# Kernel optimization log

Hardware: AMD Instinct MI355X
Metric: run time of the kernel (lower is better)

Reference implementation:

```python
import jax, jax.numpy as jnp
import numpy as np

HIDDEN = 2048
N_HEADS = 16
HEAD_DIM = HIDDEN // N_HEADS
SEQ = 4096
ROPE_BASE = 10000.0


def setup_inputs() -> dict:
    key = jax.random.key(0)
    ks = jax.random.split(key, 5)
    sc = 1.0 / np.sqrt(HIDDEN)
    return {
        "hidden_states": jax.random.normal(ks[0], (SEQ, HIDDEN), jnp.float32),
        "Wq": jax.random.normal(ks[1], (HIDDEN, HIDDEN), jnp.float32) * sc,
        "Wk": jax.random.normal(ks[2], (HIDDEN, HIDDEN), jnp.float32) * sc,
        "Wv": jax.random.normal(ks[3], (HIDDEN, HIDDEN), jnp.float32) * sc,
        "Wo": jax.random.normal(ks[4], (HIDDEN, HIDDEN), jnp.float32) * sc,
    }


def _rope_cos_sin(seq_len, head_dim, dtype):
    # Llama-style rotary embedding tables, shape [S, 1, head_dim]
    inv_freq = 1.0 / (ROPE_BASE ** (jnp.arange(0, head_dim, 2, dtype=jnp.float32) / head_dim))
    pos = jnp.arange(seq_len, dtype=jnp.float32)
    freqs = pos[:, None] * inv_freq[None, :]          # [S, d/2]
    emb = jnp.concatenate([freqs, freqs], axis=-1)     # [S, d]
    return jnp.cos(emb)[:, None, :].astype(dtype), jnp.sin(emb)[:, None, :].astype(dtype)


def _rotate_half(x):
    h = x.shape[-1] // 2
    return jnp.concatenate([-x[..., h:], x[..., :h]], axis=-1)


def reference(hidden_states, Wq, Wk, Wv, Wo):
    S, H = hidden_states.shape
    d = HEAD_DIM
    # QKV projections (nn.Linear: x @ W.T), split into heads: [S, nH, d]
    q = (hidden_states @ Wq.T).reshape(S, N_HEADS, d)
    k = (hidden_states @ Wk.T).reshape(S, N_HEADS, d)
    v = (hidden_states @ Wv.T).reshape(S, N_HEADS, d)
    # Per-position RoPE on q and k
    cos, sin = _rope_cos_sin(S, d, q.dtype)
    q = q * cos + _rotate_half(q) * sin
    k = k * cos + _rotate_half(k) * sin
    # Causal scaled-dot-product attention, scores [nH, S, S]
    scores = jnp.einsum("snd,tnd->nst", q, k) / jnp.sqrt(jnp.asarray(d, q.dtype))
    causal = jnp.tril(jnp.ones((S, S), dtype=bool))
    scores = jnp.where(causal[None, :, :], scores, jnp.asarray(-1e30, scores.dtype))
    probs = jax.nn.softmax(scores, axis=-1)
    ctx = jnp.einsum("nst,tnd->snd", probs, v).reshape(S, H)
    return ctx @ Wo.T
```

## Files before the change

### kernel.cpp

```cpp
#include <hip/hip_runtime.h>

#define SEQ 4096
#define HIDDEN 2048
#define NHEADS 16
#define HDIM 128
#define QBLK 128
#define WQ 32
#define KVB 64

typedef float f32x4 __attribute__((ext_vector_type(4)));
typedef __bf16 bf16x8 __attribute__((ext_vector_type(8)));
typedef unsigned int u32x4 __attribute__((ext_vector_type(4)));
typedef unsigned int u32x2 __attribute__((ext_vector_type(2)));
typedef unsigned short u16x8 __attribute__((ext_vector_type(8)));
typedef unsigned short u16x4 __attribute__((ext_vector_type(4)));
typedef unsigned short u16;

#define SCL2 0.12751747456918851f
#define RLOG 0.2076205059304601f

__device__ __forceinline__ u16 f2bf(float f) {
  unsigned u = __float_as_uint(f);
  unsigned r = 0x7fffu + ((u >> 16) & 1u);
  return (u16)((u + r) >> 16);
}
__device__ __forceinline__ unsigned cvtpk(float a, float b) {
  unsigned r;
  asm volatile("v_cvt_pk_bf16_f32 %0, %1, %2" : "=v"(r) : "v"(a), "v"(b));
  return r;
}

__device__ __forceinline__ void gload16(const u16* g, u16* l) {
  __builtin_amdgcn_global_load_lds(
      (const __attribute__((address_space(1))) unsigned int*)g,
      (__attribute__((address_space(3))) unsigned int*)l, 16, 0, 0);
}

__global__ __launch_bounds__(256) void cvt5(const float* __restrict__ X,
    const float* __restrict__ Wq, const float* __restrict__ Wk,
    const float* __restrict__ Wv, const float* __restrict__ Wo,
    u16* __restrict__ dst) {
  const size_t SH = (size_t)SEQ * HIDDEN, HH = (size_t)HIDDEN * HIDDEN;
  size_t i = ((size_t)blockIdx.x * 256 + threadIdx.x) * 8;
  const float* src; size_t off;
  if (i < SH) { src = X; off = i; }
  else if (i < SH + HH) { src = Wq; off = i - SH; }
  else if (i < SH + 2 * HH) { src = Wk; off = i - SH - HH; }
  else if (i < SH + 3 * HH) { src = Wv; off = i - SH - 2 * HH; }
  else { src = Wo; off = i - SH - 3 * HH; }
  float4 a = *reinterpret_cast<const float4*>(src + off);
  float4 b = *reinterpret_cast<const float4*>(src + off + 4);
  u16x8 o;
  o[0] = f2bf(a.x); o[1] = f2bf(a.y); o[2] = f2bf(a.z); o[3] = f2bf(a.w);
  o[4] = f2bf(b.x); o[5] = f2bf(b.y); o[6] = f2bf(b.z); o[7] = f2bf(b.w);
  *reinterpret_cast<u32x4*>(dst + i) = __builtin_bit_cast(u32x4, o);
}

__global__ __launch_bounds__(256, 3) void gemm_qkv(const u16* __restrict__ Xb,
    const u16* __restrict__ Wqb, const u16* __restrict__ Wkb,
    const u16* __restrict__ Wvb, u16* __restrict__ Qo, u16* __restrict__ Ko,
    u16* __restrict__ Vt) {
  __shared__ u16 As[2][128 * 32];
  __shared__ u16 Bs[2][128 * 32];
  const int wg = blockIdx.x;
  const int swz = (wg & 7) * 192 + (wg >> 3);
  const int z = swz >> 9;
  const int rr_ = swz & 511;
  const u16 *A, *B;
  u16* C;
  int bm, bn, cst;
  if (z == 2) {
    A = Wvb; B = Xb; C = Vt;
    bm = (rr_ & 15) << 7; bn = (rr_ >> 4) << 7; cst = SEQ;
  } else {
    A = Xb; B = z ? Wkb : Wqb; C = z ? Ko : Qo;
    bm = (rr_ & 31) << 7; bn = (rr_ >> 5) << 7; cst = HIDDEN;
  }
  const int t = threadIdx.x, lane = t & 63, wave = t >> 6;
  const int lrow = lane & 15, lk = (lane >> 4) * 8;
  const int wr = wave * 32;
  const int r0 = t >> 2, c0 = (t & 3) * 8;

  f32x4 acc[2][8] = {};

#pragma unroll
  for (int is = 0; is < 2; ++is) {
    gload16(A + (size_t)(bm + is * 64 + r0) * HIDDEN + c0, &As[0][is * 2048 + t * 8]);
    gload16(B + (size_t)(bn + is * 64 + r0) * HIDDEN + c0, &Bs[0][is * 2048 + t * 8]);
  }
  __syncthreads();

  int p = 0;
  for (int kt = 0; kt < HIDDEN; kt += 32) {
    if (kt + 32 < HIDDEN) {
#pragma unroll
      for (int is = 0; is < 2; ++is) {
        gload16(A + (size_t)(bm + is * 64 + r0) * HIDDEN + kt + 32 + c0,
                &As[p ^ 1][is * 2048 + t * 8]);
        gload16(B + (size_t)(bn + is * 64 + r0) * HIDDEN + kt + 32 + c0,
                &Bs[p ^ 1][is * 2048 + t * 8]);
      }
    }
    bf16x8 af[2], bfv[8];
#pragma unroll
    for (int m = 0; m < 2; ++m)
      af[m] = __builtin_bit_cast(bf16x8,
          *reinterpret_cast<const u32x4*>(&As[p][(wr + m * 16 + lrow) * 32 + lk]));
#pragma unroll
    for (int n = 0; n < 8; ++n)
      bfv[n] = __builtin_bit_cast(bf16x8,
          *reinterpret_cast<const u32x4*>(&Bs[p][(n * 16 + lrow) * 32 + lk]));
#pragma unroll
    for (int n = 0; n < 8; ++n)
#pragma unroll
      for (int m = 0; m < 2; ++m)
        acc[m][n] = __builtin_amdgcn_mfma_f32_16x16x32_bf16(af[m], bfv[n], acc[m][n], 0, 0, 0);
    __syncthreads();
    p ^= 1;
  }

  const int rb = (lane >> 4) * 4;
  if (z < 2) {
#pragma unroll
    for (int m = 0; m < 2; ++m)
#pragma unroll
      for (int q = 0; q < 4; ++q) {
        const int s = bm + wr + m * 16 + rb + q;
#pragma unroll
        for (int n = 0; n < 4; ++n) {
          const int ii = n * 16 + lrow;
          float inv = exp2f((float)ii * -RLOG);
          float ang = (float)s * inv;
          float sn, cs;
          __sincosf(ang, &sn, &cs);
          float x1 = acc[m][n][q], x2 = acc[m][n + 4][q];
          acc[m][n][q] = x1 * cs - x2 * sn;
          acc[m][n + 4][q] = x2 * cs + x1 * sn;
        }
      }
  }
#pragma unroll
  for (int m = 0; m < 2; ++m)
#pragma unroll
    for (int n = 0; n < 8; ++n)
#pragma unroll
      for (int q = 0; q < 4; ++q)
        C[(size_t)(bm + wr + m * 16 + rb + q) * cst + bn + n * 16 + lrow] =
            f2bf(acc[m][n][q]);
}

__global__ __launch_bounds__(256, 3) void gemm_out(const u16* __restrict__ A,
    const u16* __restrict__ B, float* __restrict__ C) {
  __shared__ u16 As[2][128 * 32];
  __shared__ u16 Bs[2][128 * 32];
  const int wg = blockIdx.x;
  const int swz = (wg & 7) * 64 + (wg >> 3);
  const int bm = (swz & 31) << 7;
  const int bn = (swz >> 5) << 7;
  const int t = threadIdx.x, lane = t & 63, wave = t >> 6;
  const int lrow = lane & 15, lk = (lane >> 4) * 8;
  const int wr = wave * 32;
  const int r0 = t >> 2, c0 = (t & 3) * 8;

  f32x4 acc[2][8] = {};

#pragma unroll
  for (int is = 0; is < 2; ++is) {
    gload16(A + (size_t)(bm + is * 64 + r0) * HIDDEN + c0, &As[0][is * 2048 + t * 8]);
    gload16(B + (size_t)(bn + is * 64 + r0) * HIDDEN + c0, &Bs[0][is * 2048 + t * 8]);
  }
  __syncthreads();

  int p = 0;
  for (int kt = 0; kt < HIDDEN; kt += 32) {
    if (kt + 32 < HIDDEN) {
#pragma unroll
      for (int is = 0; is < 2; ++is) {
        gload16(A + (size_t)(bm + is * 64 + r0) * HIDDEN + kt + 32 + c0,
                &As[p ^ 1][is * 2048 + t * 8]);
        gload16(B + (size_t)(bn + is * 64 + r0) * HIDDEN + kt + 32 + c0,
                &Bs[p ^ 1][is * 2048 + t * 8]);
      }
    }
    bf16x8 af[2], bfv[8];
#pragma unroll
    for (int m = 0; m < 2; ++m)
      af[m] = __builtin_bit_cast(bf16x8,
          *reinterpret_cast<const u32x4*>(&As[p][(wr + m * 16 + lrow) * 32 + lk]));
#pragma unroll
    for (int n = 0; n < 8; ++n)
      bfv[n] = __builtin_bit_cast(bf16x8,
          *reinterpret_cast<const u32x4*>(&Bs[p][(n * 16 + lrow) * 32 + lk]));
#pragma unroll
    for (int n = 0; n < 8; ++n)
#pragma unroll
      for (int m = 0; m < 2; ++m)
        acc[m][n] = __builtin_amdgcn_mfma_f32_16x16x32_bf16(af[m], bfv[n], acc[m][n], 0, 0, 0);
    __syncthreads();
    p ^= 1;
  }

  const int rb = (lane >> 4) * 4;
#pragma unroll
  for (int m = 0; m < 2; ++m)
#pragma unroll
    for (int n = 0; n < 8; ++n)
#pragma unroll
      for (int q = 0; q < 4; ++q)
        C[(size_t)(bm + wr + m * 16 + rb + q) * HIDDEN + bn + n * 16 + lrow] =
            acc[m][n][q];
}

__global__ __launch_bounds__(256, 2) void attn_kernel(const u16* __restrict__ Q,
                                                      const u16* __restrict__ Kg,
                                                      const u16* __restrict__ Vt,
                                                      u16* __restrict__ O) {
  __shared__ u16 Ks[2][KVB * 128];
  __shared__ u16 Vs[2][128 * KVB];
  __shared__ u16 Ps[4][WQ * KVB];
  const int t = threadIdx.x;
  const int wave = t >> 6;
  const int lane = t & 63;
  const int lrow = lane & 15;
  const int lgrp = lane >> 4;

  const int b = blockIdx.x;
  const int j = b & 255;
  const int h = j >> 4;
  const int qtile = (b < 256) ? (31 - (j & 15)) : (j & 15);
  const int qb0 = qtile * QBLK;
  const int qw = qb0 + wave * WQ;

  bf16x8 qf[2][4];
#pragma unroll
  for (int rowf = 0; rowf < 2; ++rowf)
#pragma unroll
    for (int kk = 0; kk < 4; ++kk)
      qf[rowf][kk] = __builtin_bit_cast(bf16x8, *reinterpret_cast<const u32x4*>(
          Q + (size_t)(qw + rowf * 16 + lrow) * HIDDEN + h * HDIM + kk * 32 + lgrp * 8));

  const u16* kgb[4]; const u16* vgb[4]; int kof[4], vof[4];
#pragma unroll
  for (int is = 0; is < 4; ++is) {
    int ch = is * 256 + t;
    int krow = ch >> 4, kslot = ch & 15;
    int kcol = ((kslot & 8) | ((kslot ^ krow) & 7)) * 8;
    kgb[is] = Kg + (size_t)krow * HIDDEN + h * HDIM + kcol;
    kof[is] = ch * 8;
    int vrow = ch >> 3, vslot = ch & 7;
    int vcol = ((vslot ^ vrow) & 7) * 8;
    vgb[is] = Vt + (size_t)(h * HDIM + vrow) * SEQ + vcol;
    vof[is] = ch * 8;
  }

  f32x4 acc[2][8] = {};
  float m2[2] = {-1e30f, -1e30f};
  float lsum[2] = {0.f, 0.f};

  const int nblk = 2 * qtile + 2;

#pragma unroll
  for (int is = 0; is < 4; ++is) {
    gload16(kgb[is], &Ks[0][kof[is]]);
    gload16(vgb[is], &Vs[0][vof[is]]);
  }
  __syncthreads();

  int cur = 0;
  for (int bt = 0; bt < nblk; ++bt) {
    const int t0 = bt * KVB;
    if (bt + 1 < nblk) {
      const int t1 = t0 + KVB;
#pragma unroll
      for (int is = 0; is < 4; ++is) {
        gload16(kgb[is] + (size_t)t1 * HIDDEN, &Ks[cur ^ 1][kof[is]]);
        gload16(vgb[is] + t1, &Vs[cur ^ 1][vof[is]]);
      }
    }

    if (t0 <= qw + WQ - 1) {
      const bool need_mask = (t0 + KVB - 1 > qw);
      f32x4 sc[2][4] = {};
      __builtin_amdgcn_s_setprio(1);
#pragma unroll
      for (int kk = 0; kk < 4; ++kk) {
#pragma unroll
        for (int colf = 0; colf < 4; ++colf) {
          int trow = colf * 16 + lrow;
          int slot = kk * 4 + lgrp;
          bf16x8 kf = __builtin_bit_cast(bf16x8, *reinterpret_cast<const u32x4*>(
              &Ks[cur][trow * 128 + ((slot & 8) | ((slot ^ trow) & 7)) * 8]));
#pragma unroll
          for (int rowf = 0; rowf < 2; ++rowf)
            sc[rowf][colf] = __builtin_amdgcn_mfma_f32_16x16x32_bf16(
                kf, qf[rowf][kk], sc[rowf][colf], 0, 0, 0);
        }
      }
      __builtin_amdgcn_s_setprio(0);

      float pmax[2];
#pragma unroll
      for (int rowf = 0; rowf < 2; ++rowf) {
        const int q = qw + rowf * 16 + lrow;
        float mx = -3.0e38f;
#pragma unroll
        for (int colf = 0; colf < 4; ++colf) {
          const int kvb0 = t0 + colf * 16 + lgrp * 4;
#pragma unroll
          for (int r = 0; r < 4; ++r) {
            float v = sc[rowf][colf][r] * SCL2;
            if (need_mask) v = (kvb0 + r <= q) ? v : -1e30f;
            sc[rowf][colf][r] = v;
            mx = fmaxf(mx, v);
          }
        }
        mx = fmaxf(mx, __shfl_xor(mx, 16));
        mx = fmaxf(mx, __shfl_xor(mx, 32));
        pmax[rowf] = mx;
      }

      bool grow = (pmax[0] > m2[0] + 11.5f) || (pmax[1] > m2[1] + 11.5f);
      if (__any(grow)) {
#pragma unroll
        for (int rowf = 0; rowf < 2; ++rowf) {
          float mn = fmaxf(m2[rowf], pmax[rowf]);
          float sf = exp2f(m2[rowf] - mn);
          m2[rowf] = mn;
          lsum[rowf] *= sf;
#pragma unroll
          for (int r = 0; r < 4; ++r) {
            float sfr = __shfl(sf, (lane & 48) | (lgrp * 4 + r));
#pragma unroll
            for (int nn = 0; nn < 8; ++nn) acc[rowf][nn][r] *= sfr;
          }
        }
      }

#pragma unroll
      for (int rowf = 0; rowf < 2; ++rowf) {
        const int q = rowf * 16 + lrow;
        float ps = 0.f;
#pragma unroll
        for (int colf = 0; colf < 4; ++colf) {
          float pv[4];
#pragma unroll
          for (int r = 0; r < 4; ++r) {
            pv[r] = exp2f(sc[rowf][colf][r] - m2[rowf]);
            ps += pv[r];
          }
          u32x2 pk2;
          pk2[0] = cvtpk(pv[0], pv[1]);
          pk2[1] = cvtpk(pv[2], pv[3]);
          const int kv = colf * 16 + lgrp * 4;
          const int sw = (kv >> 3) ^ (q & 7);
          *reinterpret_cast<u32x2*>(&Ps[wave][q * 64 + sw * 8 + (kv & 7)]) = pk2;
        }
        ps += __shfl_xor(ps, 16);
        ps += __shfl_xor(ps, 32);
        lsum[rowf] += ps;
      }

      __builtin_amdgcn_s_setprio(1);
#pragma unroll
      for (int ks = 0; ks < 2; ++ks) {
        bf16x8 pa[2];
#pragma unroll
        for (int rowf = 0; rowf < 2; ++rowf) {
          const int q = rowf * 16 + lrow;
          const int sl = ks * 4 + lgrp;
          pa[rowf] = __builtin_bit_cast(bf16x8, *reinterpret_cast<const u32x4*>(
              &Ps[wave][q * 64 + (sl ^ (q & 7)) * 8]));
        }
#pragma unroll
        for (int nn = 0; nn < 8; ++nn) {
          const int d = nn * 16 + lrow;
          bf16x8 vb = __builtin_bit_cast(bf16x8, *reinterpret_cast<const u32x4*>(
              &Vs[cur][d * 64 + (((ks * 4 + lgrp) ^ d) & 7) * 8]));
#pragma unroll
          for (int rowf = 0; rowf < 2; ++rowf)
            acc[rowf][nn] = __builtin_amdgcn_mfma_f32_16x16x32_bf16(
                pa[rowf], vb, acc[rowf][nn], 0, 0, 0);
        }
      }
      __builtin_amdgcn_s_setprio(0);
    }

    __syncthreads();
    cur ^= 1;
  }

#pragma unroll
  for (int rowf = 0; rowf < 2; ++rowf) {
    float inv[4];
#pragma unroll
    for (int r = 0; r < 4; ++r) {
      float lsr = __shfl(lsum[rowf], (lane & 48) | (lgrp * 4 + r));
      inv[r] = 1.0f / lsr;
    }
#pragma unroll
    for (int nn = 0; nn < 8; ++nn)
#pragma unroll
      for (int r = 0; r < 4; ++r) {
        int row = qw + rowf * 16 + lgrp * 4 + r;
        int col = h * HDIM + nn * 16 + lrow;
        O[(size_t)row * HIDDEN + col] = f2bf(acc[rowf][nn][r] * inv[r]);
      }
  }
}

extern "C" void kernel_launch(void* const* d_in, const int* in_sizes, int n_in,
                              void* d_out, int out_size, void* d_ws, size_t ws_size,
                              hipStream_t stream) {
  const float* X  = (const float*)d_in[0];
  const float* Wq = (const float*)d_in[1];
  const float* Wk = (const float*)d_in[2];
  const float* Wv = (const float*)d_in[3];
  const float* Wo = (const float*)d_in[4];
  float* out = (float*)d_out;

  u16* ws = (u16*)d_ws;
  const size_t SH = (size_t)SEQ * HIDDEN;
  const size_t HH = (size_t)HIDDEN * HIDDEN;
  u16* Xb  = ws;
  u16* Wqb = Xb + SH;
  u16* Wkb = Wqb + HH;
  u16* Wvb = Wkb + HH;
  u16* Wob = Wvb + HH;
  u16* Qb  = Wob + HH;
  u16* Kb  = Qb + SH;
  u16* Vtb = Kb + SH;
  u16* Cb  = Vtb + SH;

  cvt5<<<(int)((SH + 4 * HH) / 2048), 256, 0, stream>>>(X, Wq, Wk, Wv, Wo, ws);

  gemm_qkv<<<1536, 256, 0, stream>>>(Xb, Wqb, Wkb, Wvb, Qb, Kb, Vtb);

  attn_kernel<<<512, 256, 0, stream>>>(Qb, Kb, Vtb, Cb);

  gemm_out<<<512, 256, 0, stream>>>(Cb, Wob, out);
}
```

Measured before the change: 376.0 us.

## Split long causal attention KV ranges across blocks and merge partials in combine kernel

Attention work for each query tile is now split along the KV dimension into 1 to 4 chunks, sized by how much causal work the tile has. The grid grows from 512 to 1280 roughly balanced blocks, which removes the tail where long, late-position tiles run alone. Split chunks write unnormalized bf16 partial outputs plus per-row max and sum to workspace that the earlier stages no longer need. A new combine kernel rescales and merges those partials. This adds an extra launch and extra global traffic for the partials, and rounds the partials to bf16 before merging.

New measurement: 384.1 us. 2.2% more time.

```diff
diff --git a/kernel.cpp b/kernel.cpp
--- a/kernel.cpp
+++ b/kernel.cpp
@@ -24,6 +24,9 @@
   unsigned r = 0x7fffu + ((u >> 16) & 1u);
   return (u16)((u + r) >> 16);
 }
+__device__ __forceinline__ float bf2f(u16 u) {
+  return __uint_as_float(((unsigned)u) << 16);
+}
 __device__ __forceinline__ unsigned cvtpk(float a, float b) {
   unsigned r;
   asm volatile("v_cvt_pk_bf16_f32 %0, %1, %2" : "=v"(r) : "v"(a), "v"(b));
@@ -34,6 +37,12 @@
   __builtin_amdgcn_global_load_lds(
       (const __attribute__((address_space(1))) unsigned int*)g,
       (__attribute__((address_space(3))) unsigned int*)l, 16, 0, 0);
+}
+
+__device__ __forceinline__ int cumq(int q) {
+  if (q < 16) return (q - 8) * 2;
+  if (q < 24) return 16 + (q - 16) * 3;
+  return 40 + (q - 24) * 4;
 }
 
 __global__ __launch_bounds__(256) void cvt5(const float* __restrict__ X,
@@ -214,7 +223,9 @@
 __global__ __launch_bounds__(256, 2) void attn_kernel(const u16* __restrict__ Q,
                                                       const u16* __restrict__ Kg,
                                                       const u16* __restrict__ Vt,
-                                                      u16* __restrict__ O) {
+                                                      u16* __restrict__ O,
+                                                      u16* __restrict__ Opart,
+                                                      float* __restrict__ Ml) {
   __shared__ u16 Ks[2][KVB * 128];
   __shared__ u16 Vs[2][128 * KVB];
   __shared__ u16 Ps[4][WQ * KVB];
@@ -224,11 +235,20 @@
   const int lrow = lane & 15;
   const int lgrp = lane >> 4;
 
-  const int b = blockIdx.x;
-  const int j = b & 255;
-  const int h = j >> 4;
-  const int qtile = (b < 256) ? (31 - (j & 15)) : (j & 15);
-  const int qb0 = qtile * QBLK;
+  const int g = blockIdx.x;
+  const int h = g / 80;
+  const int e = 79 - (g - h * 80);
+  int q, c, nc;
+  if (e < 8)       { q = e;               c = 0;            nc = 1; }
+  else if (e < 24) { q = 8 + ((e - 8) >> 1);  c = (e - 8) & 1;  nc = 2; }
+  else if (e < 48) { q = 16 + (e - 24) / 3;   c = (e - 24) % 3; nc = 3; }
+  else             { q = 24 + ((e - 48) >> 2); c = (e - 48) & 3; nc = 4; }
+  const int total = 2 * q + 2;
+  const int base = total / nc, rem = total - base * nc;
+  const int it0 = c * base + (c < rem ? c : rem);
+  const int it1 = it0 + base + (c < rem ? 1 : 0);
+
+  const int qb0 = q * QBLK;
   const int qw = qb0 + wave * WQ;
 
   bf16x8 qf[2][4];
@@ -257,20 +277,18 @@
   float m2[2] = {-1e30f, -1e30f};
   float lsum[2] = {0.f, 0.f};
 
-  const int nblk = 2 * qtile + 2;
-
 #pragma unroll
   for (int is = 0; is < 4; ++is) {
-    gload16(kgb[is], &Ks[0][kof[is]]);
-    gload16(vgb[is], &Vs[0][vof[is]]);
+    gload16(kgb[is] + (size_t)(it0 * KVB) * HIDDEN, &Ks[0][kof[is]]);
+    gload16(vgb[is] + it0 * KVB, &Vs[0][vof[is]]);
   }
   __syncthreads();
 
   int cur = 0;
-  for (int bt = 0; bt < nblk; ++bt) {
+  for (int bt = it0; bt < it1; ++bt) {
     const int t0 = bt * KVB;
-    if (bt + 1 < nblk) {
-      const int t1 = t0 + KVB;
+    if (bt + 1 < it1) {
+      const int t1 = (bt + 1) * KVB;
 #pragma unroll
       for (int is = 0; is < 4; ++is) {
         gload16(kgb[is] + (size_t)t1 * HIDDEN, &Ks[cur ^ 1][kof[is]]);
@@ -301,7 +319,7 @@
       float pmax[2];
 #pragma unroll
       for (int rowf = 0; rowf < 2; ++rowf) {
-        const int q = qw + rowf * 16 + lrow;
+        const int qg = qw + rowf * 16 + lrow;
         float mx = -3.0e38f;
 #pragma unroll
         for (int colf = 0; colf < 4; ++colf) {
@@ -309,7 +327,7 @@
 #pragma unroll
           for (int r = 0; r < 4; ++r) {
             float v = sc[rowf][colf][r] * SCL2;
-            if (need_mask) v = (kvb0 + r <= q) ? v : -1e30f;
+            if (need_mask) v = (kvb0 + r <= qg) ? v : -1e30f;
             sc[rowf][colf][r] = v;
             mx = fmaxf(mx, v);
           }
@@ -338,7 +356,7 @@
 
 #pragma unroll
       for (int rowf = 0; rowf < 2; ++rowf) {
-        const int q = rowf * 16 + lrow;
+        const int qq = rowf * 16 + lrow;
         float ps = 0.f;
 #pragma unroll
         for (int colf = 0; colf < 4; ++colf) {
@@ -352,8 +370,8 @@
           pk2[0] = cvtpk(pv[0], pv[1]);
           pk2[1] = cvtpk(pv[2], pv[3]);
           const int kv = colf * 16 + lgrp * 4;
-          const int sw = (kv >> 3) ^ (q & 7);
-          *reinterpret_cast<u32x2*>(&Ps[wave][q * 64 + sw * 8 + (kv & 7)]) = pk2;
+          const int sw = (kv >> 3) ^ (qq & 7);
+          *reinterpret_cast<u32x2*>(&Ps[wave][qq * 64 + sw * 8 + (kv & 7)]) = pk2;
         }
         ps += __shfl_xor(ps, 16);
         ps += __shfl_xor(ps, 32);
@@ -366,10 +384,10 @@
         bf16x8 pa[2];
 #pragma unroll
         for (int rowf = 0; rowf < 2; ++rowf) {
-          const int q = rowf * 16 + lrow;
+          const int qq = rowf * 16 + lrow;
           const int sl = ks * 4 + lgrp;
           pa[rowf] = __builtin_bit_cast(bf16x8, *reinterpret_cast<const u32x4*>(
-              &Ps[wave][q * 64 + (sl ^ (q & 7)) * 8]));
+              &Ps[wave][qq * 64 + (sl ^ (qq & 7)) * 8]));
         }
 #pragma unroll
         for (int nn = 0; nn < 8; ++nn) {
@@ -389,22 +407,84 @@
     cur ^= 1;
   }
 
-#pragma unroll
-  for (int rowf = 0; rowf < 2; ++rowf) {
-    float inv[4];
-#pragma unroll
-    for (int r = 0; r < 4; ++r) {
-      float lsr = __shfl(lsum[rowf], (lane & 48) | (lgrp * 4 + r));
-      inv[r] = 1.0f / lsr;
-    }
-#pragma unroll
-    for (int nn = 0; nn < 8; ++nn)
+  if (nc == 1) {
+#pragma unroll
+    for (int rowf = 0; rowf < 2; ++rowf) {
+      float inv[4];
 #pragma unroll
       for (int r = 0; r < 4; ++r) {
-        int row = qw + rowf * 16 + lgrp * 4 + r;
-        int col = h * HDIM + nn * 16 + lrow;
-        O[(size_t)row * HIDDEN + col] = f2bf(acc[rowf][nn][r] * inv[r]);
-      }
+        float lsr = __shfl(lsum[rowf], (lane & 48) | (lgrp * 4 + r));
+        inv[r] = 1.0f / lsr;
+      }
+#pragma unroll
+      for (int nn = 0; nn < 8; ++nn)
+#pragma unroll
+        for (int r = 0; r < 4; ++r) {
+          int row = qw + rowf * 16 + lgrp * 4 + r;
+          int col = h * HDIM + nn * 16 + lrow;
+          O[(size_t)row * HIDDEN + col] = f2bf(acc[rowf][nn][r] * inv[r]);
+        }
+    }
+  } else {
+    const int slot = h * 72 + cumq(q) + c;
+    u16* Op = Opart + (size_t)slot * (QBLK * HDIM);
+    float* ml = Ml + (size_t)slot * 256;
+#pragma unroll
+    for (int rowf = 0; rowf < 2; ++rowf) {
+#pragma unroll
+      for (int nn = 0; nn < 8; ++nn)
+#pragma unroll
+        for (int r = 0; r < 4; ++r) {
+          int rl = wave * 32 + rowf * 16 + lgrp * 4 + r;
+          Op[rl * HDIM + nn * 16 + lrow] = f2bf(acc[rowf][nn][r]);
+        }
+      if (lgrp == 0) {
+        int rl = wave * 32 + rowf * 16 + lrow;
+        ml[rl] = m2[rowf];
+        ml[128 + rl] = lsum[rowf];
+      }
+    }
+  }
+}
+
+__global__ __launch_bounds__(256) void combine_kernel(const u16* __restrict__ Opart,
+                                                      const float* __restrict__ Ml,
+                                                      u16* __restrict__ O) {
+  const int bid = blockIdx.x;
+  const int h = bid / 24;
+  const int q = 8 + bid % 24;
+  const int nc = q / 8 + 1;
+  const int sbase = h * 72 + cumq(q);
+  const int r = threadIdx.x >> 1;
+  const int d0 = (threadIdx.x & 1) * 64;
+
+  float w[4], l = 0.f, M = -3.0e38f;
+#pragma unroll
+  for (int c = 0; c < 4; ++c)
+    if (c < nc) M = fmaxf(M, Ml[(size_t)(sbase + c) * 256 + r]);
+#pragma unroll
+  for (int c = 0; c < 4; ++c)
+    if (c < nc) {
+      w[c] = exp2f(Ml[(size_t)(sbase + c) * 256 + r] - M);
+      l += w[c] * Ml[(size_t)(sbase + c) * 256 + 128 + r];
+    }
+  const float inv = 1.0f / l;
+
+  for (int dd = 0; dd < 64; dd += 8) {
+    float a8[8] = {};
+#pragma unroll
+    for (int c = 0; c < 4; ++c)
+      if (c < nc) {
+        u16x8 v = *reinterpret_cast<const u16x8*>(
+            Opart + (size_t)(sbase + c) * (QBLK * HDIM) + r * HDIM + d0 + dd);
+#pragma unroll
+        for (int j = 0; j < 8; ++j) a8[j] += w[c] * bf2f(v[j]);
+      }
+    u16x8 o8;
+#pragma unroll
+    for (int j = 0; j < 8; ++j) o8[j] = f2bf(a8[j] * inv);
+    *reinterpret_cast<u16x8*>(
+        &O[(size_t)(q * QBLK + r) * HIDDEN + h * HDIM + d0 + dd]) = o8;
   }
 }
 
@@ -431,11 +511,15 @@
   u16* Vtb = Kb + SH;
   u16* Cb  = Vtb + SH;
 
+  u16* Opart = ws;
+  float* Ml = (float*)(ws + (size_t)1152 * 16384);
+
   cvt5<<<(int)((SH + 4 * HH) / 2048), 256, 0, stream>>>(X, Wq, Wk, Wv, Wo, ws);
 
   gemm_qkv<<<1536, 256, 0, stream>>>(Xb, Wqb, Wkb, Wvb, Qb, Kb, Vtb);
 
-  attn_kernel<<<512, 256, 0, stream>>>(Qb, Kb, Vtb, Cb);
+  attn_kernel<<<1280, 256, 0, stream>>>(Qb, Kb, Vtb, Cb, Opart, Ml);
+  combine_kernel<<<384, 256, 0, stream>>>(Opart, Ml, Cb);
 
   gemm_out<<<512, 256, 0, stream>>>(Cb, Wob, out);
 }
```
